# Optimization experiments

Hardware: AMD Instinct MI355X
Metric: run time of the kernel (lower is better)

Reference implementation:

```python
import jax, jax.numpy as jnp
import numpy as np

N, B, D, A, E, H = 8, 32768, 128, 64, 32, 128


def setup_inputs() -> dict:
    key = jax.random.key(0)
    ks = jax.random.split(key, 22)
    g = lambda k, shape: (jax.random.normal(k, shape, dtype=jnp.float32) * 0.1)
    return {
        "states": jax.random.normal(ks[0], (N, B, D), dtype=jnp.float32),
        # per-agent DQN (2-hidden-layer MLP), stacked over agents
        "W1": g(ks[1], (N, D, H)), "b1": g(ks[2], (N, H)),
        "W2": g(ks[3], (N, H, H)), "b2": g(ks[4], (N, H)),
        "W3": g(ks[5], (N, H, A)), "b3": g(ks[6], (N, A)),
        # per-agent query MLP
        "Wq1": g(ks[7], (N, D, E)), "bq1": g(ks[8], (N, E)),
        "Wq2": g(ks[9], (N, E, E)), "bq2": g(ks[10], (N, E)),
        # per-agent key Linear
        "Wk": g(ks[11], (N, D, E)), "bk": g(ks[12], (N, E)),
        # shared scaling MLP (D->1->1)
        "Ws1": g(ks[13], (D, 1)), "bs1": g(ks[14], (1,)),
        "Ws2": g(ks[15], (1, 1)), "bs2": g(ks[16], (1,)),
        # shared constraint MLP (D->E->1)
        "Wc1": g(ks[17], (D, E)), "bc1": g(ks[18], (E,)),
        "Wc2": g(ks[19], (E, 1)), "bc2": g(ks[20], (1,)),
    }


def reference(states, W1, b1, W2, b2, W3, b3, Wq1, bq1, Wq2, bq2, Wk, bk,
              Ws1, bs1, Ws2, bs2, Wc1, bc1, Wc2, bc2):
    relu = jax.nn.relu
    # per-agent DQN -> q_values [B, N, A]
    h = relu(jnp.einsum('nbd,ndh->nbh', states, W1) + b1[:, None, :])
    h = relu(jnp.einsum('nbh,nhk->nbk', h, W2) + b2[:, None, :])
    q_values = (jnp.einsum('nbh,nha->nba', h, W3) + b3[:, None, :]).transpose(1, 0, 2)
    # per-agent keys [B, N, E]
    keys = (jnp.einsum('nbd,nde->nbe', states, Wk) + bk[:, None, :]).transpose(1, 0, 2)
    # per-agent queries [B, N, E]
    qh = relu(jnp.einsum('nbd,nde->nbe', states, Wq1) + bq1[:, None, :])
    queries = (jnp.einsum('nbe,nef->nbf', qh, Wq2) + bq2[:, None, :]).transpose(1, 0, 2)
    # attention [B, N, N]
    scores = jnp.einsum('bnd,bmd->bnm', queries, keys) / jnp.sqrt(jnp.float32(E))
    attn = jax.nn.softmax(scores, axis=-1)
    # faithful to original einsum 'bnm,bna->bna' (sums attn over m)
    weighted_qs = jnp.einsum('bnm,bna->bna', attn, q_values)
    # shared scaling MLP, sigmoid gate [B, N, 1]
    s = relu(jnp.einsum('nbd,do->nbo', states, Ws1) + bs1)
    s = jnp.einsum('nbo,op->nbp', s, Ws2) + bs2
    scaling = jax.nn.sigmoid(s.transpose(1, 0, 2))
    summed_q = jnp.mean(scaling * weighted_qs, axis=1)  # [B, A]
    # shared constraint MLP [B, N, 1] -> mean over agents [B, 1]
    c = relu(jnp.einsum('nbd,de->nbe', states, Wc1) + bc1)
    c = (jnp.einsum('nbe,eo->nbo', c, Wc2) + bc2).transpose(1, 0, 2)
    c = jnp.mean(c, axis=1)
    return summed_q + c  # [B, A]
```

## Files before the change

kernel.cpp:

```cpp
#include <hip/hip_runtime.h>
#include <hip/hip_bf16.h>

#define NAG 8
#define BATCH 32768
#define DDIM 128
#define ADIM 64
#define HDIM 128

#define NJ1 11
#define NJ2 8
#define NJ3 4
#define FB_L1 (NJ1*4)
#define FB_L2 (NJ2*4)
#define FB_L3 (NJ3*4)
#define FB_B  (FB_L2+FB_L3)
#define FB_TOT (FB_L1+FB_L2+FB_L3)
#define WAGENT (FB_TOT*512)

typedef __attribute__((ext_vector_type(8))) short bf16x8;
typedef __attribute__((ext_vector_type(4))) float f32x4;
typedef __attribute__((ext_vector_type(4))) unsigned int u32x4;

static __device__ __forceinline__ unsigned short f2bf(float f) {
  unsigned int u = __builtin_bit_cast(unsigned int, f);
  u += 0x7fffu + ((u >> 16) & 1u);
  return (unsigned short)(u >> 16);
}

static __device__ __forceinline__ unsigned int cvt_pk_bf16(float a, float b) {
  unsigned int r;
  asm("v_cvt_pk_bf16_f32 %0, %1, %2" : "=v"(r) : "v"(a), "v"(b));
  return r;
}

static __device__ __forceinline__ void gload_lds16(const void* g, void* l) {
  __builtin_amdgcn_global_load_lds(
      (const __attribute__((address_space(1))) unsigned int*)g,
      (__attribute__((address_space(3))) unsigned int*)l, 16, 0, 0);
}

__global__ void __launch_bounds__(256)
prep_weights(const float* __restrict__ W1, const float* __restrict__ W2,
             const float* __restrict__ W3, const float* __restrict__ Wc1,
             const float* __restrict__ Ws1, const float* __restrict__ b1,
             const float* __restrict__ bc1, const float* __restrict__ bs1,
             unsigned short* __restrict__ wbuf, float* __restrict__ b1e)
{
  int tid = blockIdx.x * 256 + threadIdx.x;
  if (tid < NAG * WAGENT) {
    int agent = tid / WAGENT;
    int rem   = tid % WAGENT;
    int fb = rem >> 9;
    int li = rem & 511;
    int l = li >> 3, t = li & 7;
    int lr = l & 15, lg = l >> 4;
    float v = 0.0f;
    if (fb < FB_L1) {
      int j = fb >> 2, kk = fb & 3;
      int col = j*16 + lr, k = kk*32 + lg*8 + t;
      if (col < 128)       v = W1[((size_t)agent*128 + k)*128 + col];
      else if (col < 160)  v = Wc1[k*32 + (col-128)];
      else if (col == 160) v = Ws1[k];
    } else if (fb < FB_L1 + FB_L2) {
      int f = fb - FB_L1;
      int j = f >> 2, kk = f & 3;
      int col = j*16 + lr, k = kk*32 + lg*8 + t;
      v = W2[((size_t)agent*128 + k)*128 + col];
    } else {
      int f = fb - FB_L1 - FB_L2;
      int j = f >> 2, kk = f & 3;
      int col = j*16 + lr, k = kk*32 + lg*8 + t;
      v = W3[((size_t)agent*128 + k)*64 + col];
    }
    wbuf[tid] = f2bf(v);
  }
  if (tid < NAG * 176) {
    int agent = tid / 176, col = tid % 176;
    float v = 0.0f;
    if (col < 128)       v = b1[agent*128 + col];
    else if (col < 160)  v = bc1[col - 128];
    else if (col == 160) v = bs1[0];
    b1e[tid] = v;
  }
}

__global__ void __launch_bounds__(256, 2)
qatten_main(const float* __restrict__ states,
            const float* __restrict__ b2g, const float* __restrict__ b3g,
            const float* __restrict__ ws2p, const float* __restrict__ bs2p,
            const float* __restrict__ wc2g, const float* __restrict__ bc2p,
            const unsigned short* __restrict__ wbuf,
            const float* __restrict__ b1e,
            float* __restrict__ out)
{
  __shared__ __align__(16) unsigned short bufW[FB_B*512];
  __shared__ __align__(16) unsigned short hlds[4 * 2048];

  const int tid  = threadIdx.x;
  const int wave = tid >> 6;
  const int lane = tid & 63;
  const int lr   = lane & 15;
  const int lg   = lane >> 4;
  const int row0 = blockIdx.x * 64 + wave * 16;

  unsigned short* hp = hlds + wave * 2048;

  const float ws2  = ws2p[0];
  const float bs2v = bs2p[0];
  const float bc2v = bc2p[0];
  const float wc2a = wc2g[lr];
  const float wc2b = wc2g[16 + lr];

  const f32x4 zero4 = {0.f, 0.f, 0.f, 0.f};

  f32x4 out_acc[NJ3];
#pragma unroll
  for (int j = 0; j < NJ3; ++j) out_acc[j] = zero4;

  {
    const char* sA = (const char*)wbuf;
    for (int c = wave; c < FB_L1; c += 4)
      gload_lds16(sA + c*1024 + lane*16, (char*)bufW + c*1024);
  }

  f32x4 sreg[8];
  float b1n[NJ1], b2n[NJ2], b3n[NJ3];
  {
    const float* sb = states + (size_t)row0 * DDIM;
#pragma unroll
    for (int kk = 0; kk < 4; ++kk) {
      const float* p = sb + lr*DDIM + kk*32 + lg*8;
      sreg[kk*2]   = *(const f32x4*)p;
      sreg[kk*2+1] = *(const f32x4*)(p + 4);
    }
#pragma unroll
    for (int j = 0; j < NJ1; ++j) b1n[j] = b1e[j*16 + lr];
#pragma unroll
    for (int j = 0; j < NJ2; ++j) b2n[j] = b2g[j*16 + lr];
#pragma unroll
    for (int j = 0; j < NJ3; ++j) b3n[j] = b3g[j*16 + lr];
  }
  __syncthreads();

  for (int a = 0; a < NAG; ++a) {
    float b1v[NJ1], b2v[NJ2], b3v[NJ3];
#pragma unroll
    for (int j = 0; j < NJ1; ++j) b1v[j] = b1n[j];
#pragma unroll
    for (int j = 0; j < NJ2; ++j) b2v[j] = b2n[j];
#pragma unroll
    for (int j = 0; j < NJ3; ++j) b3v[j] = b3n[j];

    bf16x8 afr[4];
#pragma unroll
    for (int kk = 0; kk < 4; ++kk) {
      f32x4 v0 = sreg[kk*2], v1 = sreg[kk*2+1];
      u32x4 w;
      w[0] = cvt_pk_bf16(v0[0], v0[1]);
      w[1] = cvt_pk_bf16(v0[2], v0[3]);
      w[2] = cvt_pk_bf16(v1[0], v1[1]);
      w[3] = cvt_pk_bf16(v1[2], v1[3]);
      afr[kk] = __builtin_bit_cast(bf16x8, w);
    }

    if (a < NAG-1) {
      const float* sb = states + ((size_t)(a+1) * BATCH + row0) * DDIM;
#pragma unroll
      for (int kk = 0; kk < 4; ++kk) {
        const float* p = sb + lr*DDIM + kk*32 + lg*8;
        sreg[kk*2]   = *(const f32x4*)p;
        sreg[kk*2+1] = *(const f32x4*)(p + 4);
      }
    }

    f32x4 eacc[3];
    {
      bf16x8 pf[3][4];
#pragma unroll
      for (int kk = 0; kk < 4; ++kk) {
        pf[0][kk] = *(const bf16x8*)&bufW[(0*4 + kk)*512 + lane*8];
        pf[1][kk] = *(const bf16x8*)&bufW[(1*4 + kk)*512 + lane*8];
      }
#pragma unroll
      for (int j = 0; j < 11; ++j) {
        if (j + 2 <= 10) {
#pragma unroll
          for (int kk = 0; kk < 4; ++kk)
            pf[(j+2)%3][kk] = *(const bf16x8*)&bufW[((j+2)*4 + kk)*512 + lane*8];
        }
        f32x4 acc = zero4;
#pragma unroll
        for (int kk = 0; kk < 4; ++kk)
          acc = __builtin_amdgcn_mfma_f32_16x16x32_bf16(afr[kk], pf[j%3][kk], acc, 0, 0, 0);
        if (j < 8) {
#pragma unroll
          for (int r = 0; r < 4; ++r) {
            float hv = acc[r] + b1v[j];
            hv = hv > 0.f ? hv : 0.f;
            int row = lg*4 + r;
            int bo = row*256 + (((j*16 + lr)*2) ^ ((row & 7) << 4));
            *(unsigned short*)((char*)hp + bo) = f2bf(hv);
          }
        } else {
          eacc[j-8] = acc;
        }
      }
    }

    float scl[4], crow[4];
#pragma unroll
    for (int r = 0; r < 4; ++r) {
      float c0 = eacc[0][r] + b1v[8];  c0 = c0 > 0.f ? c0 : 0.f;
      float c1 = eacc[1][r] + b1v[9];  c1 = c1 > 0.f ? c1 : 0.f;
      float cd = c0*wc2a + c1*wc2b;
      cd += __shfl_xor(cd, 1);
      cd += __shfl_xor(cd, 2);
      cd += __shfl_xor(cd, 4);
      cd += __shfl_xor(cd, 8);
      crow[r] = cd + bc2v;
      float sp = eacc[2][r] + b1v[10];
      sp = __shfl(sp, lane & 48);
      sp = sp > 0.f ? sp : 0.f;
      float s = ws2 * sp + bs2v;
      scl[r] = 1.f / (1.f + __expf(-s));
    }

#pragma unroll
    for (int kk = 0; kk < 4; ++kk) {
      int row = lr;
      int bo = row*256 + ((kk*64 + lg*16) ^ ((row & 7) << 4));
      afr[kk] = *(const bf16x8*)((char*)hp + bo);
    }

    __syncthreads();

    {
      const char* sB = (const char*)(wbuf + (size_t)a*WAGENT + FB_L1*512);
      for (int c = wave; c < FB_B; c += 4)
        gload_lds16(sB + c*1024 + lane*16, (char*)bufW + c*1024);
    }
    if (a < NAG-1) {
#pragma unroll
      for (int j = 0; j < NJ1; ++j) b1n[j] = b1e[(a+1)*176 + j*16 + lr];
#pragma unroll
      for (int j = 0; j < NJ2; ++j) b2n[j] = b2g[(a+1)*HDIM + j*16 + lr];
#pragma unroll
      for (int j = 0; j < NJ3; ++j) b3n[j] = b3g[(a+1)*ADIM + j*16 + lr];
    }

    __syncthreads();

    {
      bf16x8 pf[3][4];
#pragma unroll
      for (int kk = 0; kk < 4; ++kk) {
        pf[0][kk] = *(const bf16x8*)&bufW[(0*4 + kk)*512 + lane*8];
        pf[1][kk] = *(const bf16x8*)&bufW[(1*4 + kk)*512 + lane*8];
      }
#pragma unroll
      for (int j = 0; j < 8; ++j) {
        if (j + 2 <= 7) {
#pragma unroll
          for (int kk = 0; kk < 4; ++kk)
            pf[(j+2)%3][kk] = *(const bf16x8*)&bufW[((j+2)*4 + kk)*512 + lane*8];
        }
        f32x4 acc = zero4;
#pragma unroll
        for (int kk = 0; kk < 4; ++kk)
          acc = __builtin_amdgcn_mfma_f32_16x16x32_bf16(afr[kk], pf[j%3][kk], acc, 0, 0, 0);
#pragma unroll
        for (int r = 0; r < 4; ++r) {
          float hv = acc[r] + b2v[j];
          hv = hv > 0.f ? hv : 0.f;
          int row = lg*4 + r;
          int bo = row*256 + (((j*16 + lr)*2) ^ ((row & 7) << 4));
          *(unsigned short*)((char*)hp + bo) = f2bf(hv);
        }
      }
    }

#pragma unroll
    for (int kk = 0; kk < 4; ++kk) {
      int row = lr;
      int bo = row*256 + ((kk*64 + lg*16) ^ ((row & 7) << 4));
      afr[kk] = *(const bf16x8*)((char*)hp + bo);
    }

    {
      bf16x8 pf[2][4];
#pragma unroll
      for (int kk = 0; kk < 4; ++kk)
        pf[0][kk] = *(const bf16x8*)&bufW[(FB_L2 + kk)*512 + lane*8];
#pragma unroll
      for (int j = 0; j < NJ3; ++j) {
        if (j < NJ3-1) {
#pragma unroll
          for (int kk = 0; kk < 4; ++kk)
            pf[(j+1)&1][kk] = *(const bf16x8*)&bufW[(FB_L2 + (j+1)*4 + kk)*512 + lane*8];
        }
        f32x4 acc = zero4;
#pragma unroll
        for (int kk = 0; kk < 4; ++kk)
          acc = __builtin_amdgcn_mfma_f32_16x16x32_bf16(afr[kk], pf[j&1][kk], acc, 0, 0, 0);
#pragma unroll
        for (int r = 0; r < 4; ++r)
          out_acc[j][r] += scl[r] * (acc[r] + b3v[j]) + crow[r];
      }
    }

    __syncthreads();

    if (a < NAG-1) {
      const char* sA = (const char*)(wbuf + (size_t)(a+1)*WAGENT);
      for (int c = wave; c < FB_L1; c += 4)
        gload_lds16(sA + c*1024 + lane*16, (char*)bufW + c*1024);
    }

    __syncthreads();
  }

#pragma unroll
  for (int j = 0; j < NJ3; ++j)
#pragma unroll
    for (int r = 0; r < 4; ++r) {
      size_t row = (size_t)row0 + lg*4 + r;
      out[row*ADIM + j*16 + lr] = out_acc[j][r] * 0.125f;
    }
}

extern "C" void kernel_launch(void* const* d_in, const int* in_sizes, int n_in,
                              void* d_out, int out_size, void* d_ws, size_t ws_size,
                              hipStream_t stream)
{
  const float* states = (const float*)d_in[0];
  const float* W1  = (const float*)d_in[1];
  const float* b1  = (const float*)d_in[2];
  const float* W2  = (const float*)d_in[3];
  const float* b2  = (const float*)d_in[4];
  const float* W3  = (const float*)d_in[5];
  const float* b3  = (const float*)d_in[6];
  const float* Ws1 = (const float*)d_in[13];
  const float* bs1 = (const float*)d_in[14];
  const float* Ws2 = (const float*)d_in[15];
  const float* bs2 = (const float*)d_in[16];
  const float* Wc1 = (const float*)d_in[17];
  const float* bc1 = (const float*)d_in[18];
  const float* Wc2 = (const float*)d_in[19];
  const float* bc2 = (const float*)d_in[20];

  unsigned short* wbuf = (unsigned short*)d_ws;
  float* b1e = (float*)((char*)d_ws + (size_t)NAG * WAGENT * 2);

  dim3 pb(256), pg((NAG * WAGENT + 255) / 256);
  prep_weights<<<pg, pb, 0, stream>>>(W1, W2, W3, Wc1, Ws1, b1, bc1, bs1, wbuf, b1e);

  dim3 mb(256), mg(BATCH / 64);
  qatten_main<<<mg, mb, 0, stream>>>(states, b2, b3, Ws2, bs2, Wc2, bc2,
                                     wbuf, b1e, (float*)d_out);
}
```

Measured before the change: 61.50 us.

## Split weight LDS buffers and pipeline next-agent weight loads behind layer compute

Splits the shared-memory weight buffer into a main buffer (layer1/layer2) and a separate layer-3 buffer. The next agent's layer-1 weights are now loaded while layer 3 runs, and layer-3 weights are loaded during the next agent's layers. Layer 2 is split in two halves with partial vmcnt waits so compute can start before all weights arrive. It also uses a two-deep register prefetch instead of three-deep and a hardware bf16 convert instead of manual rounding. These remove barrier stalls on weight loads, at the cost of finer synchronization whose vmcnt counts must stay correct.

```diff
diff --git a/kernel.cpp b/kernel.cpp
--- a/kernel.cpp
+++ b/kernel.cpp
@@ -13,7 +13,6 @@
 #define FB_L1 (NJ1*4)
 #define FB_L2 (NJ2*4)
 #define FB_L3 (NJ3*4)
-#define FB_B  (FB_L2+FB_L3)
 #define FB_TOT (FB_L1+FB_L2+FB_L3)
 #define WAGENT (FB_TOT*512)
 
@@ -31,6 +30,12 @@
   unsigned int r;
   asm("v_cvt_pk_bf16_f32 %0, %1, %2" : "=v"(r) : "v"(a), "v"(b));
   return r;
+}
+
+static __device__ __forceinline__ unsigned short f2bf1(float f) {
+  unsigned int r;
+  asm("v_cvt_pk_bf16_f32 %0, %1, %2" : "=v"(r) : "v"(f), "v"(f));
+  return (unsigned short)r;
 }
 
 static __device__ __forceinline__ void gload_lds16(const void* g, void* l) {
@@ -93,7 +98,8 @@
             const float* __restrict__ b1e,
             float* __restrict__ out)
 {
-  __shared__ __align__(16) unsigned short bufW[FB_B*512];
+  __shared__ __align__(16) unsigned short bufMain[FB_L1*512];
+  __shared__ __align__(16) unsigned short bufL3[FB_L3*512];
   __shared__ __align__(16) unsigned short hlds[4 * 2048];
 
   const int tid  = threadIdx.x;
@@ -118,9 +124,18 @@
   for (int j = 0; j < NJ3; ++j) out_acc[j] = zero4;
 
   {
-    const char* sA = (const char*)wbuf;
-    for (int c = wave; c < FB_L1; c += 4)
-      gload_lds16(sA + c*1024 + lane*16, (char*)bufW + c*1024);
+    const char* s0 = (const char*)wbuf;
+    for (int t = wave; t < NJ1; t += 4)
+#pragma unroll
+      for (int c = 0; c < 4; ++c)
+        gload_lds16(s0 + (t*4+c)*1024 + lane*16, (char*)bufMain + (t*4+c)*1024);
+    const char* s3 = s0 + (size_t)(FB_L1+FB_L2)*1024;
+    {
+      int t = wave;
+#pragma unroll
+      for (int c = 0; c < 4; ++c)
+        gload_lds16(s3 + (t*4+c)*1024 + lane*16, (char*)bufL3 + (t*4+c)*1024);
+    }
   }
 
   f32x4 sreg[8];
@@ -175,23 +190,21 @@
 
     f32x4 eacc[3];
     {
-      bf16x8 pf[3][4];
-#pragma unroll
-      for (int kk = 0; kk < 4; ++kk) {
-        pf[0][kk] = *(const bf16x8*)&bufW[(0*4 + kk)*512 + lane*8];
-        pf[1][kk] = *(const bf16x8*)&bufW[(1*4 + kk)*512 + lane*8];
-      }
+      bf16x8 pf[2][4];
+#pragma unroll
+      for (int kk = 0; kk < 4; ++kk)
+        pf[0][kk] = *(const bf16x8*)&bufMain[kk*512 + lane*8];
 #pragma unroll
       for (int j = 0; j < 11; ++j) {
-        if (j + 2 <= 10) {
+        if (j < 10) {
 #pragma unroll
           for (int kk = 0; kk < 4; ++kk)
-            pf[(j+2)%3][kk] = *(const bf16x8*)&bufW[((j+2)*4 + kk)*512 + lane*8];
+            pf[(j+1)&1][kk] = *(const bf16x8*)&bufMain[((j+1)*4 + kk)*512 + lane*8];
         }
         f32x4 acc = zero4;
 #pragma unroll
         for (int kk = 0; kk < 4; ++kk)
-          acc = __builtin_amdgcn_mfma_f32_16x16x32_bf16(afr[kk], pf[j%3][kk], acc, 0, 0, 0);
+          acc = __builtin_amdgcn_mfma_f32_16x16x32_bf16(afr[kk], pf[j&1][kk], acc, 0, 0, 0);
         if (j < 8) {
 #pragma unroll
           for (int r = 0; r < 4; ++r) {
@@ -199,7 +212,7 @@
             hv = hv > 0.f ? hv : 0.f;
             int row = lg*4 + r;
             int bo = row*256 + (((j*16 + lr)*2) ^ ((row & 7) << 4));
-            *(unsigned short*)((char*)hp + bo) = f2bf(hv);
+            *(unsigned short*)((char*)hp + bo) = f2bf1(hv);
           }
         } else {
           eacc[j-8] = acc;
@@ -235,46 +248,71 @@
     __syncthreads();
 
     {
-      const char* sB = (const char*)(wbuf + (size_t)a*WAGENT + FB_L1*512);
-      for (int c = wave; c < FB_B; c += 4)
-        gload_lds16(sB + c*1024 + lane*16, (char*)bufW + c*1024);
-    }
-    if (a < NAG-1) {
-#pragma unroll
-      for (int j = 0; j < NJ1; ++j) b1n[j] = b1e[(a+1)*176 + j*16 + lr];
-#pragma unroll
-      for (int j = 0; j < NJ2; ++j) b2n[j] = b2g[(a+1)*HDIM + j*16 + lr];
-#pragma unroll
-      for (int j = 0; j < NJ3; ++j) b3n[j] = b3g[(a+1)*ADIM + j*16 + lr];
-    }
-
-    __syncthreads();
-
-    {
-      bf16x8 pf[3][4];
-#pragma unroll
-      for (int kk = 0; kk < 4; ++kk) {
-        pf[0][kk] = *(const bf16x8*)&bufW[(0*4 + kk)*512 + lane*8];
-        pf[1][kk] = *(const bf16x8*)&bufW[(1*4 + kk)*512 + lane*8];
-      }
-#pragma unroll
-      for (int j = 0; j < 8; ++j) {
-        if (j + 2 <= 7) {
+      const char* s2 = (const char*)(wbuf + (size_t)a*WAGENT + FB_L1*512);
+      for (int t = wave; t < NJ2; t += 4)
+#pragma unroll
+        for (int c = 0; c < 4; ++c)
+          gload_lds16(s2 + (t*4+c)*1024 + lane*16, (char*)bufMain + (t*4+c)*1024);
+    }
+
+    asm volatile("s_waitcnt vmcnt(4)" ::: "memory");
+    __builtin_amdgcn_s_barrier();
+    __builtin_amdgcn_sched_barrier(0);
+
+    {
+      bf16x8 pf[2][4];
+#pragma unroll
+      for (int kk = 0; kk < 4; ++kk)
+        pf[0][kk] = *(const bf16x8*)&bufMain[kk*512 + lane*8];
+#pragma unroll
+      for (int j = 0; j < 4; ++j) {
+        if (j < 3) {
 #pragma unroll
           for (int kk = 0; kk < 4; ++kk)
-            pf[(j+2)%3][kk] = *(const bf16x8*)&bufW[((j+2)*4 + kk)*512 + lane*8];
+            pf[(j+1)&1][kk] = *(const bf16x8*)&bufMain[((j+1)*4 + kk)*512 + lane*8];
         }
         f32x4 acc = zero4;
 #pragma unroll
         for (int kk = 0; kk < 4; ++kk)
-          acc = __builtin_amdgcn_mfma_f32_16x16x32_bf16(afr[kk], pf[j%3][kk], acc, 0, 0, 0);
+          acc = __builtin_amdgcn_mfma_f32_16x16x32_bf16(afr[kk], pf[j&1][kk], acc, 0, 0, 0);
 #pragma unroll
         for (int r = 0; r < 4; ++r) {
           float hv = acc[r] + b2v[j];
           hv = hv > 0.f ? hv : 0.f;
           int row = lg*4 + r;
           int bo = row*256 + (((j*16 + lr)*2) ^ ((row & 7) << 4));
-          *(unsigned short*)((char*)hp + bo) = f2bf(hv);
+          *(unsigned short*)((char*)hp + bo) = f2bf1(hv);
+        }
+      }
+    }
+
+    asm volatile("s_waitcnt vmcnt(0)" ::: "memory");
+    __builtin_amdgcn_s_barrier();
+    __builtin_amdgcn_sched_barrier(0);
+
+    {
+      bf16x8 pf[2][4];
+#pragma unroll
+      for (int kk = 0; kk < 4; ++kk)
+        pf[0][kk] = *(const bf16x8*)&bufMain[(4*4 + kk)*512 + lane*8];
+#pragma unroll
+      for (int j = 4; j < 8; ++j) {
+        if (j < 7) {
+#pragma unroll
+          for (int kk = 0; kk < 4; ++kk)
+            pf[(j+1)&1][kk] = *(const bf16x8*)&bufMain[((j+1)*4 + kk)*512 + lane*8];
+        }
+        f32x4 acc = zero4;
+#pragma unroll
+        for (int kk = 0; kk < 4; ++kk)
+          acc = __builtin_amdgcn_mfma_f32_16x16x32_bf16(afr[kk], pf[j&1][kk], acc, 0, 0, 0);
+#pragma unroll
+        for (int r = 0; r < 4; ++r) {
+          float hv = acc[r] + b2v[j];
+          hv = hv > 0.f ? hv : 0.f;
+          int row = lg*4 + r;
+          int bo = row*256 + (((j*16 + lr)*2) ^ ((row & 7) << 4));
+          *(unsigned short*)((char*)hp + bo) = f2bf1(hv);
         }
       }
     }
@@ -286,17 +324,33 @@
       afr[kk] = *(const bf16x8*)((char*)hp + bo);
     }
 
+    __syncthreads();
+
+    if (a < NAG-1) {
+      const char* sA = (const char*)(wbuf + (size_t)(a+1)*WAGENT);
+      for (int t = wave; t < NJ1; t += 4)
+#pragma unroll
+        for (int c = 0; c < 4; ++c)
+          gload_lds16(sA + (t*4+c)*1024 + lane*16, (char*)bufMain + (t*4+c)*1024);
+#pragma unroll
+      for (int j = 0; j < NJ1; ++j) b1n[j] = b1e[(a+1)*176 + j*16 + lr];
+#pragma unroll
+      for (int j = 0; j < NJ2; ++j) b2n[j] = b2g[(a+1)*HDIM + j*16 + lr];
+#pragma unroll
+      for (int j = 0; j < NJ3; ++j) b3n[j] = b3g[(a+1)*ADIM + j*16 + lr];
+    }
+
     {
       bf16x8 pf[2][4];
 #pragma unroll
       for (int kk = 0; kk < 4; ++kk)
-        pf[0][kk] = *(const bf16x8*)&bufW[(FB_L2 + kk)*512 + lane*8];
+        pf[0][kk] = *(const bf16x8*)&bufL3[kk*512 + lane*8];
 #pragma unroll
       for (int j = 0; j < NJ3; ++j) {
         if (j < NJ3-1) {
 #pragma unroll
           for (int kk = 0; kk < 4; ++kk)
-            pf[(j+1)&1][kk] = *(const bf16x8*)&bufW[(FB_L2 + (j+1)*4 + kk)*512 + lane*8];
+            pf[(j+1)&1][kk] = *(const bf16x8*)&bufL3[((j+1)*4 + kk)*512 + lane*8];
         }
         f32x4 acc = zero4;
 #pragma unroll
@@ -311,12 +365,12 @@
     __syncthreads();
 
     if (a < NAG-1) {
-      const char* sA = (const char*)(wbuf + (size_t)(a+1)*WAGENT);
-      for (int c = wave; c < FB_L1; c += 4)
-        gload_lds16(sA + c*1024 + lane*16, (char*)bufW + c*1024);
-    }
-
-    __syncthreads();
+      const char* s3 = (const char*)(wbuf + (size_t)(a+1)*WAGENT + (size_t)(FB_L1+FB_L2)*512);
+      int t = wave;
+#pragma unroll
+      for (int c = 0; c < 4; ++c)
+        gload_lds16(s3 + (t*4+c)*1024 + lane*16, (char*)bufL3 + (t*4+c)*1024);
+    }
   }
 
 #pragma unroll
```

Measured after the change: 63.95 us. 4.0% more time.

## Load extra L1 and L3 weight fragments from global into registers, shrink LDS buffer

Applied to the files above, without the earlier changes.

The extra layer-1 columns (constraint and scaling heads) and the layer-3 weights are now read directly from global into register fragments instead of being staged through LDS. This lets the LDS weight buffer shrink to 32 chunks, which may raise occupancy, and lets the next agent's layer-1 prefetch start before the layer-3 MFMAs instead of after a barrier. Bias prefetching into registers is replaced by per-agent loads issued near their use, and bf16 stores use the hardware convert instruction. The change raises VGPR pressure with up to 28 extra bf16x8 fragments live, and the direct global loads may stall MFMAs if their latency is not hidden.

```diff
diff --git a/kernel.cpp b/kernel.cpp
--- a/kernel.cpp
+++ b/kernel.cpp
@@ -11,9 +11,9 @@
 #define NJ2 8
 #define NJ3 4
 #define FB_L1 (NJ1*4)
+#define FB_L1M 32
 #define FB_L2 (NJ2*4)
 #define FB_L3 (NJ3*4)
-#define FB_B  (FB_L2+FB_L3)
 #define FB_TOT (FB_L1+FB_L2+FB_L3)
 #define WAGENT (FB_TOT*512)
 
@@ -31,6 +31,12 @@
   unsigned int r;
   asm("v_cvt_pk_bf16_f32 %0, %1, %2" : "=v"(r) : "v"(a), "v"(b));
   return r;
+}
+
+static __device__ __forceinline__ unsigned short f2bf1(float f) {
+  unsigned int r;
+  asm("v_cvt_pk_bf16_f32 %0, %1, %2" : "=v"(r) : "v"(f), "v"(f));
+  return (unsigned short)r;
 }
 
 static __device__ __forceinline__ void gload_lds16(const void* g, void* l) {
@@ -93,7 +99,7 @@
             const float* __restrict__ b1e,
             float* __restrict__ out)
 {
-  __shared__ __align__(16) unsigned short bufW[FB_B*512];
+  __shared__ __align__(16) unsigned short bufW[FB_L1M*512];
   __shared__ __align__(16) unsigned short hlds[4 * 2048];
 
   const int tid  = threadIdx.x;
@@ -119,12 +125,11 @@
 
   {
     const char* sA = (const char*)wbuf;
-    for (int c = wave; c < FB_L1; c += 4)
+    for (int c = wave; c < FB_L1M; c += 4)
       gload_lds16(sA + c*1024 + lane*16, (char*)bufW + c*1024);
   }
 
   f32x4 sreg[8];
-  float b1n[NJ1], b2n[NJ2], b3n[NJ3];
   {
     const float* sb = states + (size_t)row0 * DDIM;
 #pragma unroll
@@ -133,23 +138,19 @@
       sreg[kk*2]   = *(const f32x4*)p;
       sreg[kk*2+1] = *(const f32x4*)(p + 4);
     }
-#pragma unroll
-    for (int j = 0; j < NJ1; ++j) b1n[j] = b1e[j*16 + lr];
-#pragma unroll
-    for (int j = 0; j < NJ2; ++j) b2n[j] = b2g[j*16 + lr];
-#pragma unroll
-    for (int j = 0; j < NJ3; ++j) b3n[j] = b3g[j*16 + lr];
   }
   __syncthreads();
 
   for (int a = 0; a < NAG; ++a) {
-    float b1v[NJ1], b2v[NJ2], b3v[NJ3];
-#pragma unroll
-    for (int j = 0; j < NJ1; ++j) b1v[j] = b1n[j];
-#pragma unroll
-    for (int j = 0; j < NJ2; ++j) b2v[j] = b2n[j];
-#pragma unroll
-    for (int j = 0; j < NJ3; ++j) b3v[j] = b3n[j];
+    bf16x8 gfr[3][4];
+    {
+      const unsigned short* wg = wbuf + (size_t)a*WAGENT + (size_t)FB_L1M*512;
+#pragma unroll
+      for (int t = 0; t < 3; ++t)
+#pragma unroll
+        for (int kk = 0; kk < 4; ++kk)
+          gfr[t][kk] = *(const bf16x8*)&wg[(t*4+kk)*512 + lane*8];
+    }
 
     bf16x8 afr[4];
 #pragma unroll
@@ -173,7 +174,9 @@
       }
     }
 
-    f32x4 eacc[3];
+    float b1v[NJ1];
+#pragma unroll
+    for (int j = 0; j < NJ1; ++j) b1v[j] = b1e[a*176 + j*16 + lr];
     {
       bf16x8 pf[3][4];
 #pragma unroll
@@ -182,8 +185,8 @@
         pf[1][kk] = *(const bf16x8*)&bufW[(1*4 + kk)*512 + lane*8];
       }
 #pragma unroll
-      for (int j = 0; j < 11; ++j) {
-        if (j + 2 <= 10) {
+      for (int j = 0; j < 8; ++j) {
+        if (j + 2 <= 7) {
 #pragma unroll
           for (int kk = 0; kk < 4; ++kk)
             pf[(j+2)%3][kk] = *(const bf16x8*)&bufW[((j+2)*4 + kk)*512 + lane*8];
@@ -192,19 +195,25 @@
 #pragma unroll
         for (int kk = 0; kk < 4; ++kk)
           acc = __builtin_amdgcn_mfma_f32_16x16x32_bf16(afr[kk], pf[j%3][kk], acc, 0, 0, 0);
-        if (j < 8) {
-#pragma unroll
-          for (int r = 0; r < 4; ++r) {
-            float hv = acc[r] + b1v[j];
-            hv = hv > 0.f ? hv : 0.f;
-            int row = lg*4 + r;
-            int bo = row*256 + (((j*16 + lr)*2) ^ ((row & 7) << 4));
-            *(unsigned short*)((char*)hp + bo) = f2bf(hv);
-          }
-        } else {
-          eacc[j-8] = acc;
+#pragma unroll
+        for (int r = 0; r < 4; ++r) {
+          float hv = acc[r] + b1v[j];
+          hv = hv > 0.f ? hv : 0.f;
+          int row = lg*4 + r;
+          int bo = row*256 + (((j*16 + lr)*2) ^ ((row & 7) << 4));
+          *(unsigned short*)((char*)hp + bo) = f2bf1(hv);
         }
       }
+    }
+
+    f32x4 eacc[3];
+#pragma unroll
+    for (int jx = 0; jx < 3; ++jx) {
+      f32x4 acc = zero4;
+#pragma unroll
+      for (int kk = 0; kk < 4; ++kk)
+        acc = __builtin_amdgcn_mfma_f32_16x16x32_bf16(afr[kk], gfr[jx][kk], acc, 0, 0, 0);
+      eacc[jx] = acc;
     }
 
     float scl[4], crow[4];
@@ -236,21 +245,26 @@
 
     {
       const char* sB = (const char*)(wbuf + (size_t)a*WAGENT + FB_L1*512);
-      for (int c = wave; c < FB_B; c += 4)
+      for (int c = wave; c < FB_L2; c += 4)
         gload_lds16(sB + c*1024 + lane*16, (char*)bufW + c*1024);
     }
-    if (a < NAG-1) {
-#pragma unroll
-      for (int j = 0; j < NJ1; ++j) b1n[j] = b1e[(a+1)*176 + j*16 + lr];
-#pragma unroll
-      for (int j = 0; j < NJ2; ++j) b2n[j] = b2g[(a+1)*HDIM + j*16 + lr];
-#pragma unroll
-      for (int j = 0; j < NJ3; ++j) b3n[j] = b3g[(a+1)*ADIM + j*16 + lr];
-    }
 
     __syncthreads();
 
-    {
+    bf16x8 lfr[4][4];
+    {
+      const unsigned short* w3 = wbuf + (size_t)a*WAGENT + (size_t)(FB_L1+FB_L2)*512;
+#pragma unroll
+      for (int t = 0; t < 4; ++t)
+#pragma unroll
+        for (int kk = 0; kk < 4; ++kk)
+          lfr[t][kk] = *(const bf16x8*)&w3[(t*4+kk)*512 + lane*8];
+    }
+
+    {
+      float b2v[NJ2];
+#pragma unroll
+      for (int j = 0; j < NJ2; ++j) b2v[j] = b2g[a*HDIM + j*16 + lr];
       bf16x8 pf[3][4];
 #pragma unroll
       for (int kk = 0; kk < 4; ++kk) {
@@ -274,7 +288,7 @@
           hv = hv > 0.f ? hv : 0.f;
           int row = lg*4 + r;
           int bo = row*256 + (((j*16 + lr)*2) ^ ((row & 7) << 4));
-          *(unsigned short*)((char*)hp + bo) = f2bf(hv);
+          *(unsigned short*)((char*)hp + bo) = f2bf1(hv);
         }
       }
     }
@@ -286,34 +300,28 @@
       afr[kk] = *(const bf16x8*)((char*)hp + bo);
     }
 
-    {
-      bf16x8 pf[2][4];
-#pragma unroll
-      for (int kk = 0; kk < 4; ++kk)
-        pf[0][kk] = *(const bf16x8*)&bufW[(FB_L2 + kk)*512 + lane*8];
+    __syncthreads();
+
+    if (a < NAG-1) {
+      const char* sA = (const char*)(wbuf + (size_t)(a+1)*WAGENT);
+      for (int c = wave; c < FB_L1M; c += 4)
+        gload_lds16(sA + c*1024 + lane*16, (char*)bufW + c*1024);
+    }
+
+    {
+      float b3v[NJ3];
+#pragma unroll
+      for (int j = 0; j < NJ3; ++j) b3v[j] = b3g[a*ADIM + j*16 + lr];
 #pragma unroll
       for (int j = 0; j < NJ3; ++j) {
-        if (j < NJ3-1) {
-#pragma unroll
-          for (int kk = 0; kk < 4; ++kk)
-            pf[(j+1)&1][kk] = *(const bf16x8*)&bufW[(FB_L2 + (j+1)*4 + kk)*512 + lane*8];
-        }
         f32x4 acc = zero4;
 #pragma unroll
         for (int kk = 0; kk < 4; ++kk)
-          acc = __builtin_amdgcn_mfma_f32_16x16x32_bf16(afr[kk], pf[j&1][kk], acc, 0, 0, 0);
+          acc = __builtin_amdgcn_mfma_f32_16x16x32_bf16(afr[kk], lfr[j][kk], acc, 0, 0, 0);
 #pragma unroll
         for (int r = 0; r < 4; ++r)
           out_acc[j][r] += scl[r] * (acc[r] + b3v[j]) + crow[r];
       }
-    }
-
-    __syncthreads();
-
-    if (a < NAG-1) {
-      const char* sA = (const char*)(wbuf + (size_t)(a+1)*WAGENT);
-      for (int c = wave; c < FB_L1; c += 4)
-        gload_lds16(sA + c*1024 + lane*16, (char*)bufW + c*1024);
     }
 
     __syncthreads();
```

After: 70.82 us. 15.2% more time.
